# Kernel optimization log

Measured on AMD Instinct MI355X. Metric: run time of the kernel, lower is better.

Reference implementation:

```python
import jax, jax.numpy as jnp
import numpy as np
import math

IMG = 640.0
SIZES = [32.0, 64.0, 128.0, 256.0]
STRIDES = [4, 8, 16, 32]
ARS = [0.5, 1.0, 2.0]
PRE_TOPK = 1000      # RPN_PRE_NMS_TOPK_TEST
POST_TOPK = 150      # RPN_POST_NMS_TOPK_TEST
NMS_THR = 0.7        # RPN_NMS_THRESHOLD
MIN_SIZE = 4.0       # MIN_BOX_SIZE
BBOX_CLAMP = math.log(1000.0 / 16.0)
ROI_OUT = 7          # ROI_OUTPUT_SIZE


def conv(x, w, b, pad):
    y = jax.lax.conv_general_dilated(x, w, (1, 1), [(pad, pad), (pad, pad)],
                                     dimension_numbers=('NCHW', 'OIHW', 'NCHW'))
    return y + b[None, :, None, None]


def level_anchors(H, W, stride, size):
    sx = (jnp.arange(W, dtype=jnp.float32) + 0.5) * stride
    sy = (jnp.arange(H, dtype=jnp.float32) + 0.5) * stride
    SY, SX = jnp.meshgrid(sy, sx, indexing='ij')
    shifts = jnp.stack([SX, SY, SX, SY], axis=-1).reshape(-1, 4)  # [H*W,4]
    base = []
    area = size * size
    for ar in ARS:
        w = math.sqrt(area / ar)
        h = ar * w
        base.append([-w / 2.0, -h / 2.0, w / 2.0, h / 2.0])
    base = jnp.asarray(base, jnp.float32)  # [3,4]
    return (shifts[:, None, :] + base[None, :, :]).reshape(-1, 4)  # [H*W*3,4]


def decode(deltas, boxes):
    w = jnp.maximum(boxes[:, 2] - boxes[:, 0], 1e-6)
    h = jnp.maximum(boxes[:, 3] - boxes[:, 1], 1e-6)
    cx = boxes[:, 0] + 0.5 * w
    cy = boxes[:, 1] + 0.5 * h
    dx, dy = deltas[:, 0], deltas[:, 1]
    dw = jnp.minimum(deltas[:, 2], BBOX_CLAMP)
    dh = jnp.minimum(deltas[:, 3], BBOX_CLAMP)
    pcx = cx + dx * w
    pcy = cy + dy * h
    pw = w * jnp.exp(dw)
    ph = h * jnp.exp(dh)
    return jnp.stack([pcx - 0.5 * pw, pcy - 0.5 * ph, pcx + 0.5 * pw, pcy + 0.5 * ph], axis=1)


def pairwise_iou(b):
    area = jnp.maximum(b[:, 2] - b[:, 0], 0) * jnp.maximum(b[:, 3] - b[:, 1], 0)
    lt = jnp.maximum(b[:, None, :2], b[None, :, :2])
    rb = jnp.minimum(b[:, None, 2:], b[None, :, 2:])
    wh = jnp.maximum(rb - lt, 0.0)
    inter = wh[..., 0] * wh[..., 1]
    return inter / jnp.maximum(area[:, None] + area[None, :] - inter, 1e-6)


def roi_align(feat, boxes, scale):
    # feat [C,H,W]; boxes [R,4] in image coords; one bilinear sample per bin center
    C, H, W = feat.shape
    b = boxes * scale
    x1, y1, x2, y2 = b[:, 0], b[:, 1], b[:, 2], b[:, 3]
    bw = jnp.maximum(x2 - x1, 1.0)
    bh = jnp.maximum(y2 - y1, 1.0)
    g = (jnp.arange(ROI_OUT, dtype=jnp.float32) + 0.5) / ROI_OUT
    px = x1[:, None] + g[None, :] * bw[:, None]   # [R,7]
    py = y1[:, None] + g[None, :] * bh[:, None]
    Y = jnp.broadcast_to(py[:, :, None], (py.shape[0], ROI_OUT, ROI_OUT))
    X = jnp.broadcast_to(px[:, None, :], (px.shape[0], ROI_OUT, ROI_OUT))
    y0f = jnp.floor(Y)
    x0f = jnp.floor(X)
    ly = Y - y0f
    lx = X - x0f
    y0 = jnp.clip(y0f, 0, H - 1).astype(jnp.int32)
    y1i = jnp.clip(y0f + 1, 0, H - 1).astype(jnp.int32)
    x0 = jnp.clip(x0f, 0, W - 1).astype(jnp.int32)
    x1i = jnp.clip(x0f + 1, 0, W - 1).astype(jnp.int32)
    f = lambda yi, xi: feat[:, yi, xi]  # [C,R,7,7]
    val = (f(y0, x0) * (1 - ly) * (1 - lx) + f(y0, x1i) * (1 - ly) * lx
           + f(y1i, x0) * ly * (1 - lx) + f(y1i, x1i) * ly * lx)
    return val.transpose(1, 0, 2, 3)  # [R,C,7,7]


def _forward(p2, p3, p4, p5, rpn_conv_w, rpn_conv_b, obj_w, obj_b, delta_w, delta_b,
             fc1_w, fc1_b, fc2_w, fc2_b, cls_w, cls_b, bbox_w, bbox_b):
    feats = [p2, p3, p4, p5]
    all_boxes, all_scores, all_lvl = [], [], []
    for lvl, (feat, stride, size) in enumerate(zip(feats, STRIDES, SIZES)):
        hid = jax.nn.relu(conv(feat, rpn_conv_w, rpn_conv_b, 1))
        obj = conv(hid, obj_w, obj_b, 0)      # [1,3,H,W]
        dlt = conv(hid, delta_w, delta_b, 0)  # [1,12,H,W]
        _, A, H, W = obj.shape
        scores = obj.transpose(0, 2, 3, 1).reshape(-1)  # [H*W*3]
        deltas = dlt.reshape(1, A, 4, H, W).transpose(0, 3, 4, 1, 2).reshape(-1, 4)
        anchors = level_anchors(H, W, stride, size)
        top_s, idx = jax.lax.top_k(scores, PRE_TOPK)
        boxes = jnp.clip(decode(deltas[idx], anchors[idx]), 0.0, IMG - 1.0)
        ww = boxes[:, 2] - boxes[:, 0]
        hh = boxes[:, 3] - boxes[:, 1]
        valid = (ww >= MIN_SIZE) & (hh >= MIN_SIZE)
        all_boxes.append(boxes)
        all_scores.append(jnp.where(valid, top_s, -1e30))
        all_lvl.append(jnp.full((PRE_TOPK,), float(lvl), jnp.float32))
    boxes = jnp.concatenate(all_boxes)   # [4000,4]
    scores = jnp.concatenate(all_scores)
    lvls = jnp.concatenate(all_lvl)
    N = boxes.shape[0]
    order = jnp.argsort(-scores)
    boxes_s = boxes[order]
    scores_s = scores[order]
    lvl_s = lvls[order]
    # batched NMS: offset per level so different levels never suppress each other
    off_boxes = boxes_s + (lvl_s * (IMG + 1.0) * 2.0)[:, None]
    iou = pairwise_iou(off_boxes)
    idx_r = jnp.arange(N)

    def body(i, keep):
        sup = (iou[i] > NMS_THR) & (idx_r > i) & keep[i]
        return keep & (~sup)

    keep = jax.lax.fori_loop(0, N, body, jnp.ones((N,), bool))
    kept_scores = jnp.where(keep, scores_s, -1e30)
    _, top_idx = jax.lax.top_k(kept_scores, POST_TOPK)
    props = boxes_s[top_idx]  # [150,4]
    # FPN level assignment (canonical formula) for ROI pooling
    pw = jnp.maximum(props[:, 2] - props[:, 0], 0.0)
    ph = jnp.maximum(props[:, 3] - props[:, 1], 0.0)
    k = jnp.clip(jnp.floor(4.0 + jnp.log2(jnp.sqrt(pw * ph) / 224.0 + 1e-6)), 2, 5)
    pooled = jnp.zeros((POST_TOPK, p2.shape[1], ROI_OUT, ROI_OUT), props.dtype)
    for lvl, (feat, stride) in enumerate(zip(feats, STRIDES)):
        pl = roi_align(feat[0], props, 1.0 / stride)
        pooled = pooled + jnp.where((k == (lvl + 2))[:, None, None, None], pl, 0.0)
    x = pooled.reshape(POST_TOPK, -1)            # [150, 12544]
    x = jax.nn.relu(x @ fc1_w.T + fc1_b)
    x = jax.nn.relu(x @ fc2_w.T + fc2_b)
    cls = x @ cls_w.T + cls_b                    # [150, 21]
    bbx = x @ bbox_w.T + bbox_b                  # [150, 84]
    return jnp.concatenate([cls, bbx], axis=-1)  # [150, 105]


def setup_inputs() -> dict:
    key = jax.random.key(0)
    ks = jax.random.split(key, 14)
    C = 256
    rn = lambda k, shape, s: jax.random.normal(k, shape, jnp.float32) * s
    return {
        'p2': rn(ks[0], (1, C, 160, 160), 0.5),
        'p3': rn(ks[1], (1, C, 80, 80), 0.5),
        'p4': rn(ks[2], (1, C, 40, 40), 0.5),
        'p5': rn(ks[3], (1, C, 20, 20), 0.5),
        'rpn_conv_w': rn(ks[4], (C, C, 3, 3), 0.01),
        'rpn_conv_b': jnp.zeros((C,), jnp.float32),
        'obj_w': rn(ks[5], (3, C, 1, 1), 0.01),
        'obj_b': jnp.zeros((3,), jnp.float32),
        'delta_w': rn(ks[6], (12, C, 1, 1), 0.01),
        'delta_b': jnp.zeros((12,), jnp.float32),
        'fc1_w': rn(ks[7], (1024, C * ROI_OUT * ROI_OUT), 0.01),
        'fc1_b': jnp.zeros((1024,), jnp.float32),
        'fc2_w': rn(ks[8], (1024, 1024), 0.01),
        'fc2_b': jnp.zeros((1024,), jnp.float32),
        'cls_w': rn(ks[9], (21, 1024), 0.01),
        'cls_b': jnp.zeros((21,), jnp.float32),
        'bbox_w': rn(ks[10], (84, 1024), 0.001),
        'bbox_b': jnp.zeros((84,), jnp.float32),
    }


def reference(p2, p3, p4, p5, rpn_conv_w, rpn_conv_b, obj_w, obj_b, delta_w, delta_b,
              fc1_w, fc1_b, fc2_w, fc2_b, cls_w, cls_b, bbox_w, bbox_b):
    return _forward(p2, p3, p4, p5, rpn_conv_w, rpn_conv_b, obj_w, obj_b, delta_w, delta_b,
                    fc1_w, fc1_b, fc2_w, fc2_b, cls_w, cls_b, bbox_w, bbox_b)
```

## Files before the change

kernel.cpp:

```cpp
#include <hip/hip_runtime.h>
#include <cstdint>

typedef unsigned long long u64;
typedef unsigned int u32;

__device__ inline u32 fmono(float f){ u32 u = __float_as_uint(f); u32 m = (u & 0x80000000u) ? 0xFFFFFFFFu : 0x80000000u; return u ^ m; }

__device__ const int    g_H[4]       = {160, 80, 40, 20};
__device__ const int    g_strideI[4] = {4, 8, 16, 32};
__device__ const float  g_size[4]    = {32.f, 64.f, 128.f, 256.f};
__device__ const int    g_cofs[4]    = {0, 76800, 96000, 100800};
__device__ const int    g_cnt[4]     = {76800, 19200, 4800, 1200};
__device__ const int    c_blkBase[5] = {0, 1600, 2000, 2288, 2416};
__device__ const int    c_S[4]       = {4, 4, 8, 8};
__device__ const int    c_pofs[4]    = {0, 25600, 32000, 33600};
__device__ const size_t c_partofs[4] = {0, 26214400, 32768000, 36044800};

__global__ __launch_bounds__(256) void wtr_k(const float* __restrict__ w, float* __restrict__ wT){
  __shared__ float tile[32][33];
  int tx = threadIdx.x & 31, ty = threadIdx.x >> 5;
  int row0 = blockIdx.x*32, co0 = blockIdx.y*32;
  #pragma unroll
  for (int r=0;r<4;r++){
    int co = co0 + ty + r*8;
    tile[ty+r*8][tx] = w[(size_t)co*2304 + row0 + tx];
  }
  __syncthreads();
  #pragma unroll
  for (int r=0;r<4;r++){
    int row = row0 + ty + r*8;
    wT[(size_t)row*256 + co0 + tx] = tile[tx][ty+r*8];
  }
}

__global__ void wcat_k(const float* __restrict__ cls_w, const float* __restrict__ cls_b,
                       const float* __restrict__ bbox_w, const float* __restrict__ bbox_b,
                       float* __restrict__ wcat, float* __restrict__ bcat){
  int t = blockIdx.x*256 + threadIdx.x;
  if (t < 105*1024){ int o = t >> 10, k = t & 1023; wcat[t] = (o < 21) ? cls_w[o*1024+k] : bbox_w[(o-21)*1024+k]; }
  if (t < 105) bcat[t] = (t < 21) ? cls_b[t] : bbox_b[t-21];
}

#define KC 4
__global__ __launch_bounds__(256) void rpn_conv_all_k(
    const float* __restrict__ p0, const float* __restrict__ p1,
    const float* __restrict__ p2f, const float* __restrict__ p3f,
    const float* __restrict__ wT, const float* __restrict__ bias,
    float* __restrict__ hid, float* __restrict__ convp)
{
  int bid = blockIdx.x;
  int lvl = (bid >= c_blkBase[1]) + (bid >= c_blkBase[2]) + (bid >= c_blkBase[3]);
  int local = bid - c_blkBase[lvl];
  int nz  = c_S[lvl];
  int H = g_H[lvl], W = H;
  const float* in = (lvl==0)?p0:((lvl==1)?p1:((lvl==2)?p2f:p3f));
  float* part = convp + c_partofs[lvl];
  int zb   = local % nz;
  int cb   = (local / nz) & 3;
  int tile = local / (nz*4);

  int tilesX = (W + 15) >> 4;
  int tr0 = (tile / tilesX) * 16;
  int tc0 = (tile % tilesX) * 16;
  int ciPer = 256 / nz;
  int ciBeg = zb * ciPer;
  int t   = threadIdx.x;
  int tco = t & 15, tp = t >> 4;
  int pr = (tp >> 2) * 4, pc = (tp & 3) * 4;
  int HW = H*W;

  __shared__ float sIn[KC][18][20];
  __shared__ float sW[KC*9][64];

  float* sInF = &sIn[0][0][0];
  float* sWF  = &sW[0][0];

  int   iOff[6]; int iLds[6]; bool iOk[6];
  #pragma unroll
  for (int s=0;s<6;s++){
    int e = t + s*256;
    bool a = (s<5) || (t < (KC*324 - 5*256));
    int ee = a ? e : 0;
    int c = ee/324, r2 = ee%324, row = r2/18, col = r2%18;
    int gy = tr0+row-1, gx = tc0+col-1;
    bool ok = a && ((unsigned)gy < (unsigned)H) && ((unsigned)gx < (unsigned)W);
    iOff[s] = c*HW + gy*W + gx;
    iLds[s] = c*360 + row*20 + col;
    iOk[s]  = ok;
  }
  bool iAct5 = (t < (KC*324 - 5*256));
  int wOff[3]; int wLds[3];
  #pragma unroll
  for (int s=0;s<3;s++){
    int e4 = t + s*256;
    bool a = (s<2) || (t < (KC*9*16 - 2*256));
    int ee = a ? e4 : 0;
    int row = ee>>4, c4 = (ee&15)<<2;
    wOff[s] = row*256 + cb*64 + c4;
    wLds[s] = row*64 + c4;
  }
  bool wAct2 = (t < (KC*9*16 - 2*256));

  float acc[4][16];
  #pragma unroll
  for (int o=0;o<4;o++)
    #pragma unroll
    for (int p=0;p<16;p++) acc[o][p]=0.f;

  float  ri0,ri1,ri2,ri3,ri4,ri5;
  float4 rw0,rw1,rw2;

  {
    const float* inb = in + (size_t)ciBeg*HW;
    const float* wb  = wT + (size_t)ciBeg*2304;
    ri0 = iOk[0] ? inb[iOff[0]] : 0.f;
    ri1 = iOk[1] ? inb[iOff[1]] : 0.f;
    ri2 = iOk[2] ? inb[iOff[2]] : 0.f;
    ri3 = iOk[3] ? inb[iOff[3]] : 0.f;
    ri4 = iOk[4] ? inb[iOff[4]] : 0.f;
    ri5 = iOk[5] ? inb[iOff[5]] : 0.f;
    rw0 = *(const float4*)&wb[wOff[0]];
    rw1 = *(const float4*)&wb[wOff[1]];
    if (wAct2) rw2 = *(const float4*)&wb[wOff[2]];
  }

  int ciEnd = ciBeg + ciPer;
  for (int ci0=ciBeg; ci0<ciEnd; ci0+=KC){
    sInF[iLds[0]] = ri0; sInF[iLds[1]] = ri1; sInF[iLds[2]] = ri2;
    sInF[iLds[3]] = ri3; sInF[iLds[4]] = ri4;
    if (iAct5) sInF[iLds[5]] = ri5;
    *(float4*)&sWF[wLds[0]] = rw0;
    *(float4*)&sWF[wLds[1]] = rw1;
    if (wAct2) *(float4*)&sWF[wLds[2]] = rw2;
    __syncthreads();

    if (ci0 + KC < ciEnd){
      const float* inb = in + (size_t)(ci0+KC)*HW;
      const float* wb  = wT + (size_t)(ci0+KC)*2304;
      ri0 = iOk[0] ? inb[iOff[0]] : 0.f;
      ri1 = iOk[1] ? inb[iOff[1]] : 0.f;
      ri2 = iOk[2] ? inb[iOff[2]] : 0.f;
      ri3 = iOk[3] ? inb[iOff[3]] : 0.f;
      ri4 = iOk[4] ? inb[iOff[4]] : 0.f;
      ri5 = iOk[5] ? inb[iOff[5]] : 0.f;
      rw0 = *(const float4*)&wb[wOff[0]];
      rw1 = *(const float4*)&wb[wOff[1]];
      if (wAct2) rw2 = *(const float4*)&wb[wOff[2]];
    }

    #pragma unroll
    for (int c=0;c<KC;c++){
      float rin[6][6];
      #pragma unroll
      for (int rr=0;rr<6;rr++){
        float4 a = *(const float4*)&sIn[c][pr+rr][pc];
        float2 b = *(const float2*)&sIn[c][pr+rr][pc+4];
        rin[rr][0]=a.x; rin[rr][1]=a.y; rin[rr][2]=a.z; rin[rr][3]=a.w;
        rin[rr][4]=b.x; rin[rr][5]=b.y;
      }
      #pragma unroll
      for (int k=0;k<9;k++){
        int ky=k/3, kx=k%3;
        float4 w0 = *(const float4*)&sW[c*9+k][tco*4];
        float wv[4] = {w0.x,w0.y,w0.z,w0.w};
        #pragma unroll
        for (int dr=0;dr<4;dr++)
          #pragma unroll
          for (int dc=0;dc<4;dc++){
            float iv = rin[dr+ky][dc+kx];
            int p = dr*4+dc;
            #pragma unroll
            for (int o=0;o<4;o++) acc[o][p] = fmaf(wv[o], iv, acc[o][p]);
          }
      }
    }
    __syncthreads();
  }

  int coBase = cb*64 + tco*4;
  float* pb = part + (size_t)zb*HW*256;
  #pragma unroll
  for (int dr=0;dr<4;dr++){
    int gy = tr0+pr+dr; if (gy>=H) continue;
    #pragma unroll
    for (int dc=0;dc<4;dc++){
      int gx = tc0+pc+dc; if (gx>=W) continue;
      int p = dr*4+dc;
      *(float4*)&pb[(size_t)(gy*W+gx)*256 + coBase] = make_float4(acc[0][p],acc[1][p],acc[2][p],acc[3][p]);
    }
  }
}

__global__ __launch_bounds__(256) void conv_red_all_k(const float* __restrict__ convp,
  const float* __restrict__ bias, float* __restrict__ hid)
{
  int idx = blockIdx.x*256 + threadIdx.x;
  if (idx >= 34000*256) return;
  int lvl = (idx >= 25600*256) + (idx >= 32000*256) + (idx >= 33600*256);
  int S = c_S[lvl];
  size_t base = c_partofs[lvl];
  int local = idx - c_pofs[lvl]*256;
  size_t stride = (size_t)g_H[lvl]*g_H[lvl]*256;
  float v = 0.f;
  for (int s=0;s<S;s++) v += convp[base + (size_t)s*stride + local];
  v += bias[idx & 255];
  hid[idx] = v>0.f ? v : 0.f;
}

__global__ __launch_bounds__(256) void rpn_heads_k(
  const float* __restrict__ hid, const float* __restrict__ ow, const float* __restrict__ ob,
  const float* __restrict__ dw, const float* __restrict__ db,
  float* __restrict__ scores, float* __restrict__ deltas)
{
  __shared__ float sw[15][256];
  int t = threadIdx.x;
  for (int e=t; e<15*256; e+=256){ int o=e>>8, k=e&255; sw[o][k] = (o<3)? ow[o*256+k] : dw[(o-3)*256+k]; }
  __syncthreads();
  int wv = t>>6, lane = t&63;
  #pragma unroll
  for (int i=0;i<16;i++){
    int gpx = blockIdx.x*64 + wv*16 + i;
    if (gpx >= 34000) return;
    float4 v = *(const float4*)&hid[(size_t)gpx*256 + lane*4];
    float a[15];
    #pragma unroll
    for (int o=0;o<15;o++){
      const float* w = &sw[o][lane*4];
      a[o] = w[0]*v.x + w[1]*v.y + w[2]*v.z + w[3]*v.w;
    }
    #pragma unroll
    for (int off=32; off; off>>=1)
      #pragma unroll
      for (int o=0;o<15;o++) a[o] += __shfl_xor(a[o], off, 64);
    if (lane==0){
      for (int q=0;q<3;q++) scores[gpx*3+q] = a[q] + ob[q];
      for (int q=0;q<3;q++)
        for (int j=0;j<4;j++)
          deltas[(size_t)(gpx*3+q)*4 + j] = a[3+q*4+j] + db[q*4+j];
    }
  }
}

__global__ __launch_bounds__(1024) void topk_k(
  const float* __restrict__ scores, float* __restrict__ top_s, u32* __restrict__ top_idx)
{
  int lvl = blockIdx.x;
  int base = g_cofs[lvl], N = g_cnt[lvl];
  const int K = 1000;
  __shared__ u64 sbuf[1024];
  u32* hist = (u32*)sbuf;
  __shared__ u64 shT; __shared__ int shKr; __shared__ int scnt;
  int t = threadIdx.x;
  u64 prefix = 0; int Kr = K;
  const int shifts[6] = {53,42,31,20,9,0};
  const int nbits[6]  = {11,11,11,11,11,9};
  for (int r=0;r<6;r++){
    int shift = shifts[r], nb = nbits[r];
    for (int e=t; e<2048; e+=1024) hist[e]=0;
    __syncthreads();
    int hs = shift + nb;
    for (int e=t; e<N; e+=1024){
      u64 key = ((u64)fmono(scores[base+e]) << 32) | (u32)(~(u32)e);
      bool match = (r==0) || ((key>>hs) == (prefix>>hs));
      if (match) atomicAdd(&hist[(u32)(key>>shift) & ((1u<<nb)-1u)], 1u);
    }
    __syncthreads();
    if (t==0){
      int accu=0, nbin=1<<nb;
      for (int d=nbin-1; d>=0; --d){
        int c = (int)hist[d];
        if (accu + c >= Kr){ shT = prefix | ((u64)d << shift); shKr = Kr - accu; break; }
        accu += c;
      }
    }
    __syncthreads();
    prefix = shT; Kr = shKr;
    __syncthreads();
  }
  sbuf[t] = 0;
  if (t==0) scnt = 0;
  __syncthreads();
  for (int e=t; e<N; e+=1024){
    u64 key = ((u64)fmono(scores[base+e]) << 32) | (u32)(~(u32)e);
    if (key >= prefix){ int p = atomicAdd(&scnt,1); if (p < 1024) sbuf[p]=key; }
  }
  __syncthreads();
  for (int k=2;k<=1024;k<<=1)
    for (int j=k>>1;j>0;j>>=1){
      int i = t, ixj = i^j;
      if (ixj > i){
        u64 x = sbuf[i], y = sbuf[ixj];
        bool up = ((i & k) == 0);
        bool swp = up ? (x<y) : (x>y);
        if (swp){ sbuf[i]=y; sbuf[ixj]=x; }
      }
      __syncthreads();
    }
  if (t<K){
    u64 key = sbuf[t];
    u32 idx = ~((u32)key);
    top_idx[lvl*1000+t] = idx;
    top_s[lvl*1000+t]   = scores[base + (int)idx];
  }
}

__global__ void decode_k(const u32* __restrict__ top_idx, const float* __restrict__ top_s,
                         const float* __restrict__ deltas,
                         float* __restrict__ cat_scores, float4* __restrict__ cat_boxes)
{
  int t = blockIdx.x*256 + threadIdx.x;
  if (t >= 4000) return;
  int lvl = t/1000;
  u32 idx = top_idx[t];
  float score = top_s[t];
  int W = g_H[lvl];
  int strd = g_strideI[lvl];
  float size = g_size[lvl];
  int a = (int)(idx % 3u); int pix = (int)(idx / 3u);
  int px = pix % W, py = pix / W;
  double area = (double)size*(double)size;
  double ar = (a==0)?0.5:((a==1)?1.0:2.0);
  double wd = sqrt(area/ar);
  double hd = ar*wd;
  float bx1 = (float)(-wd*0.5), by1 = (float)(-hd*0.5), bx2=(float)(wd*0.5), by2=(float)(hd*0.5);
  float sx = ((float)px + 0.5f)*(float)strd;
  float sy = ((float)py + 0.5f)*(float)strd;
  float ax1 = sx+bx1, ay1=sy+by1, ax2=sx+bx2, ay2=sy+by2;
  float w = fmaxf(ax2-ax1, 1e-6f), h = fmaxf(ay2-ay1, 1e-6f);
  float cx = ax1 + 0.5f*w, cy = ay1 + 0.5f*h;
  const float* d = &deltas[(size_t)(g_cofs[lvl] + (int)idx)*4];
  float dx = d[0], dy = d[1];
  float dwv = fminf(d[2], 4.135166556742356f);
  float dhv = fminf(d[3], 4.135166556742356f);
  float pcx = cx + dx*w, pcy = cy + dy*h;
  float pw = w*expf(dwv), ph = h*expf(dhv);
  float x1 = pcx - 0.5f*pw, y1 = pcy - 0.5f*ph, x2 = pcx + 0.5f*pw, y2 = pcy + 0.5f*ph;
  x1 = fminf(fmaxf(x1,0.f),639.f); y1 = fminf(fmaxf(y1,0.f),639.f);
  x2 = fminf(fmaxf(x2,0.f),639.f); y2 = fminf(fmaxf(y2,0.f),639.f);
  bool valid = ((x2-x1) >= 4.f) && ((y2-y1) >= 4.f);
  cat_boxes[t] = make_float4(x1,y1,x2,y2);
  cat_scores[t] = valid ? score : -1e30f;
}

__global__ __launch_bounds__(1024) void sort_k(const float* __restrict__ cat_scores, const float4* __restrict__ cat_boxes,
  float* __restrict__ scores_s, float4* __restrict__ boxes_s, float4* __restrict__ obox)
{
  __shared__ u64 s[4096];
  int t = threadIdx.x;
  for (int i=t;i<4096;i+=1024){
    u64 key = 0;
    if (i<4000) key = ((u64)fmono(cat_scores[i])<<32) | (u32)(~(u32)i);
    s[i]=key;
  }
  __syncthreads();
  for (int k=2;k<=4096;k<<=1)
    for (int j=k>>1;j>0;j>>=1){
      for (int i=t;i<4096;i+=1024){
        int ixj=i^j;
        if (ixj>i){
          u64 x=s[i], y=s[ixj];
          bool up = ((i&k)==0);
          bool swp = up ? (x<y):(x>y);
          if (swp){ s[i]=y; s[ixj]=x; }
        }
      }
      __syncthreads();
    }
  for (int r=t;r<4000;r+=1024){
    u32 o = ~((u32)s[r]);
    float4 b = cat_boxes[o];
    scores_s[r] = cat_scores[o];
    boxes_s[r] = b;
    float off = (float)(o/1000u) * 1282.0f;
    obox[r] = make_float4(b.x+off, b.y+off, b.z+off, b.w+off);
  }
}

__global__ __launch_bounds__(256) void iou_k(const float4* __restrict__ obox, u64* __restrict__ mask)
{
  int w = threadIdx.x;
  int i = blockIdx.x*4 + threadIdx.y;
  if (i >= 4000 || w >= 63) return;
  float4 bi = obox[i];
  float ai = fmaxf(bi.z-bi.x,0.f)*fmaxf(bi.w-bi.y,0.f);
  u64 bits=0;
  int c0=w*64;
  for (int l=0;l<64;l++){
    int c=c0+l;
    if (c>=4000) break;
    if (c<=i) continue;
    float4 bc = obox[c];
    float ac = fmaxf(bc.z-bc.x,0.f)*fmaxf(bc.w-bc.y,0.f);
    float ltx = fmaxf(bi.x, bc.x), lty = fmaxf(bi.y, bc.y);
    float rbx = fminf(bi.z, bc.z), rby = fminf(bi.w, bc.w);
    float wx = fmaxf(rbx-ltx,0.f), wy = fmaxf(rby-lty,0.f);
    float inter = wx*wy;
    float uni = fmaxf(ai+ac-inter, 1e-6f);
    if (inter/uni > 0.7f) bits |= (1ull<<l);
  }
  mask[(size_t)i*63 + w] = bits;
}

#define PF 32
__global__ __launch_bounds__(64) void nms_scan_k(const u64* __restrict__ mask,
   const float* __restrict__ scores_s, const float4* __restrict__ boxes_s, float4* __restrict__ props)
{
  int lane = threadIdx.x;
  bool act = lane < 63;
  const u64* mrow = mask + lane;
  u64 removed = 0;

  u64 bufA[PF], bufB[PF];
  #pragma unroll
  for (int j=0;j<PF;j++) bufA[j] = act ? mrow[(size_t)j*63] : 0ull;

  const int NG = 4000/PF;
  for (int g=0; g<NG; g+=2){
    if (g+1 < NG){
      #pragma unroll
      for (int j=0;j<PF;j++) bufB[j] = act ? mrow[(size_t)((g+1)*PF+j)*63] : 0ull;
    }
    #pragma unroll
    for (int j=0;j<PF;j++){
      int i = g*PF + j;
      u64 rm = __shfl(removed, i>>6, 64);
      bool keep = ((rm >> (i&63)) & 1ull) == 0ull;
      if (keep) removed |= bufA[j];
    }
    if (g+2 < NG){
      #pragma unroll
      for (int j=0;j<PF;j++) bufA[j] = act ? mrow[(size_t)((g+2)*PF+j)*63] : 0ull;
    }
    if (g+1 < NG){
      #pragma unroll
      for (int j=0;j<PF;j++){
        int i = (g+1)*PF + j;
        u64 rm = __shfl(removed, i>>6, 64);
        bool keep = ((rm >> (i&63)) & 1ull) == 0ull;
        if (keep) removed |= bufB[j];
      }
    }
  }

  u64 keepbits = ~removed;
  u64 selbits = 0;
  if (act){
    #pragma unroll
    for (int j=0;j<64;j++){
      int i = lane*64 + j;
      if (i < 4000 && ((keepbits>>j)&1ull) && scores_s[i] > -1e29f) selbits |= (1ull<<j);
    }
  }
  u64 validbits = 0;
  if (act){
    int nvalid = 4000 - lane*64;
    if (nvalid >= 64) validbits = ~0ull;
    else if (nvalid > 0) validbits = (1ull<<nvalid) - 1ull;
  }
  u64 nonbits = (~selbits) & validbits;

  int cntSel = __popcll(selbits);
  int incS = cntSel;
  #pragma unroll
  for (int off2=1; off2<64; off2<<=1){ int v = __shfl_up(incS, off2, 64); if (lane>=off2) incS += v; }
  int exSel = incS - cntSel;
  int totalSel = __shfl(incS, 63, 64);
  int cnt = totalSel < 150 ? totalSel : 150;

  int cntNon = __popcll(nonbits);
  int incN = cntNon;
  #pragma unroll
  for (int off2=1; off2<64; off2<<=1){ int v = __shfl_up(incN, off2, 64); if (lane>=off2) incN += v; }
  int exNon = incN - cntNon;

  if (act){
    int r = exSel;
    #pragma unroll
    for (int j=0;j<64;j++){
      if ((selbits>>j)&1ull){
        if (r < 150) props[r] = boxes_s[lane*64 + j];
        r++;
      }
    }
    int r2 = cnt + exNon;
    #pragma unroll
    for (int j=0;j<64;j++){
      if ((nonbits>>j)&1ull){
        if (r2 < 150) props[r2] = boxes_s[lane*64 + j];
        r2++;
      }
    }
  }
}

__global__ __launch_bounds__(256) void roi_k(const float* __restrict__ p2, const float* __restrict__ p3,
  const float* __restrict__ p4, const float* __restrict__ p5, const float4* __restrict__ props, float* __restrict__ x0)
{
  int roi = blockIdx.y, p = blockIdx.x, c = threadIdx.x;
  float4 b = props[roi];
  float pw = fmaxf(b.z-b.x, 0.f), ph = fmaxf(b.w-b.y, 0.f);
  float kf = floorf(4.f + log2f(sqrtf(pw*ph)/224.f + 1e-6f));
  kf = fminf(fmaxf(kf, 2.f), 5.f);
  int lvl = (int)kf - 2;
  const float* f = (lvl==0)?p2:((lvl==1)?p3:((lvl==2)?p4:p5));
  int H = g_H[lvl]; int HW = H*H;
  float scale = 1.f/(float)g_strideI[lvl];
  float x1 = b.x*scale, y1 = b.y*scale, x2 = b.z*scale, y2 = b.w*scale;
  float bw = fmaxf(x2-x1, 1.f), bh = fmaxf(y2-y1, 1.f);
  int py = p/7, px = p%7;
  float gx = ((float)px + 0.5f)/7.f;
  float gy = ((float)py + 0.5f)/7.f;
  float X = x1 + gx*bw;
  float Y = y1 + gy*bh;
  float x0f = floorf(X), y0f = floorf(Y);
  float lx = X - x0f, ly = Y - y0f;
  int xi0 = (int)fminf(fmaxf(x0f,0.f),(float)(H-1));
  int xi1 = (int)fminf(fmaxf(x0f+1.f,0.f),(float)(H-1));
  int yi0 = (int)fminf(fmaxf(y0f,0.f),(float)(H-1));
  int yi1 = (int)fminf(fmaxf(y0f+1.f,0.f),(float)(H-1));
  float v00 = f[(size_t)c*HW + yi0*H + xi0];
  float v01 = f[(size_t)c*HW + yi0*H + xi1];
  float v10 = f[(size_t)c*HW + yi1*H + xi0];
  float v11 = f[(size_t)c*HW + yi1*H + xi1];
  float val = v00*(1.f-ly)*(1.f-lx) + v01*(1.f-ly)*lx + v10*ly*(1.f-lx) + v11*ly*lx;
  x0[(size_t)roi*12544 + c*49 + p] = val;
}

__global__ __launch_bounds__(256) void fc_split_k(const float* __restrict__ X, const float* __restrict__ Wt,
  float* __restrict__ partial, int M, int N, int K, int KS)
{
  __shared__ float sx[32][33];
  __shared__ float sw[32][64];
  int t = threadIdx.x;
  int tn = t & 15, tm = t >> 4;
  int nb = blockIdx.x, mb = blockIdx.y, zb = blockIdx.z;
  int row0 = mb*32 + tm*2, col0 = nb*64 + tn*4;
  int kbeg = zb*KS, kend = kbeg + KS;
  float acc[2][4] = {{0,0,0,0},{0,0,0,0}};
  int wn = t & 63, kg = t >> 6;
  for (int k0=kbeg;k0<kend;k0+=32){
    for (int e=t;e<1024;e+=256){
      int m=e>>5, kk=e&31;
      int row=mb*32+m;
      sx[m][kk] = (row<M)? X[(size_t)row*K + k0+kk] : 0.f;
    }
    int co = nb*64+wn;
    if (co<N){
      const float* wp = &Wt[(size_t)co*K + k0 + kg*8];
      float4 va = *(const float4*)wp;
      float4 vb = *(const float4*)(wp+4);
      sw[kg*8+0][wn]=va.x; sw[kg*8+1][wn]=va.y; sw[kg*8+2][wn]=va.z; sw[kg*8+3][wn]=va.w;
      sw[kg*8+4][wn]=vb.x; sw[kg*8+5][wn]=vb.y; sw[kg*8+6][wn]=vb.z; sw[kg*8+7][wn]=vb.w;
    } else {
      #pragma unroll
      for (int j=0;j<8;j++) sw[kg*8+j][wn]=0.f;
    }
    __syncthreads();
    #pragma unroll 8
    for (int kk=0;kk<32;kk++){
      float xa = sx[tm*2+0][kk], xb = sx[tm*2+1][kk];
      float4 wv = *(const float4*)&sw[kk][tn*4];
      acc[0][0]=fmaf(xa,wv.x,acc[0][0]); acc[0][1]=fmaf(xa,wv.y,acc[0][1]);
      acc[0][2]=fmaf(xa,wv.z,acc[0][2]); acc[0][3]=fmaf(xa,wv.w,acc[0][3]);
      acc[1][0]=fmaf(xb,wv.x,acc[1][0]); acc[1][1]=fmaf(xb,wv.y,acc[1][1]);
      acc[1][2]=fmaf(xb,wv.z,acc[1][2]); acc[1][3]=fmaf(xb,wv.w,acc[1][3]);
    }
    __syncthreads();
  }
  for (int dm=0;dm<2;dm++){
    int row=row0+dm; if (row>=M) continue;
    for (int dn=0;dn<4;dn++){
      int col=col0+dn; if (col>=N) continue;
      partial[((size_t)zb*M + row)*N + col] = acc[dm][dn];
    }
  }
}

__global__ __launch_bounds__(256) void fc_reduce_k(const float* __restrict__ partial, const float* __restrict__ bias,
  float* __restrict__ Y, int M, int N, int S, int dorelu)
{
  int idx = blockIdx.x*256 + threadIdx.x;
  if (idx >= M*N) return;
  int col = idx % N;
  float v = bias[col];
  size_t stride = (size_t)M*N;
  for (int s=0;s<S;s++) v += partial[s*stride + idx];
  if (dorelu) v = fmaxf(v, 0.f);
  Y[idx] = v;
}

extern "C" void kernel_launch(void* const* d_in, const int* in_sizes, int n_in,
                              void* d_out, int out_size, void* d_ws, size_t ws_size,
                              hipStream_t stream)
{
  (void)in_sizes; (void)n_in; (void)out_size; (void)ws_size;
  const float* p[4] = {(const float*)d_in[0], (const float*)d_in[1], (const float*)d_in[2], (const float*)d_in[3]};
  const float* rpn_w = (const float*)d_in[4];
  const float* rpn_b = (const float*)d_in[5];
  const float* obj_w = (const float*)d_in[6];
  const float* obj_b = (const float*)d_in[7];
  const float* del_w = (const float*)d_in[8];
  const float* del_b = (const float*)d_in[9];
  const float* fc1_w = (const float*)d_in[10];
  const float* fc1_b = (const float*)d_in[11];
  const float* fc2_w = (const float*)d_in[12];
  const float* fc2_b = (const float*)d_in[13];
  const float* cls_w = (const float*)d_in[14];
  const float* cls_b = (const float*)d_in[15];
  const float* bbox_w= (const float*)d_in[16];
  const float* bbox_b= (const float*)d_in[17];

  char* ws = (char*)d_ws;
  size_t off = 0;
  auto alloc = [&](size_t bytes){ size_t o = off; off += (bytes + 255) & ~(size_t)255; return o; };
  float*  wT1      = (float*)(ws + alloc(589824ull*4));
  float*  hid      = (float*)(ws + alloc(34000ull*256*4));
  float*  scores   = (float*)(ws + alloc(102000ull*4));
  float*  deltas   = (float*)(ws + alloc(102000ull*16));
  float*  top_s    = (float*)(ws + alloc(4000ull*4));
  u32*    top_idx  = (u32*)  (ws + alloc(4000ull*4));
  float*  cat_sc   = (float*)(ws + alloc(4000ull*4));
  float4* cat_bx   = (float4*)(ws + alloc(4000ull*16));
  float*  scores_s = (float*)(ws + alloc(4000ull*4));
  float4* boxes_s  = (float4*)(ws + alloc(4000ull*16));
  float4* obox     = (float4*)(ws + alloc(4000ull*16));
  u64*    mask     = (u64*)  (ws + alloc(4000ull*63*8));
  float4* props    = (float4*)(ws + alloc(150ull*16));
  float*  x0       = (float*)(ws + alloc(150ull*12544*4));
  float*  x1       = (float*)(ws + alloc(150ull*1024*4));
  float*  x2       = (float*)(ws + alloc(150ull*1024*4));
  float*  wcat     = (float*)(ws + alloc(105ull*1024*4));
  float*  bcat     = (float*)(ws + alloc(105ull*4));
  float*  convp    = (float*)(ws + alloc(36864000ull*4));
  float*  partial  = hid;

  hipLaunchKernelGGL(wtr_k, dim3(72,8), dim3(256), 0, stream, rpn_w, wT1);
  hipLaunchKernelGGL(wcat_k, dim3((105*1024+255)/256), dim3(256), 0, stream, cls_w, cls_b, bbox_w, bbox_b, wcat, bcat);

  hipLaunchKernelGGL(rpn_conv_all_k, dim3(2416), dim3(256), 0, stream,
                     p[0], p[1], p[2], p[3], wT1, rpn_b, hid, convp);
  hipLaunchKernelGGL(conv_red_all_k, dim3(34000), dim3(256), 0, stream, convp, rpn_b, hid);

  hipLaunchKernelGGL(rpn_heads_k, dim3((34000+63)/64), dim3(256), 0, stream,
                     hid, obj_w, obj_b, del_w, del_b, scores, deltas);
  hipLaunchKernelGGL(topk_k, dim3(4), dim3(1024), 0, stream, scores, top_s, top_idx);
  hipLaunchKernelGGL(decode_k, dim3(16), dim3(256), 0, stream, top_idx, top_s, deltas, cat_sc, cat_bx);
  hipLaunchKernelGGL(sort_k, dim3(1), dim3(1024), 0, stream, cat_sc, cat_bx, scores_s, boxes_s, obox);
  hipLaunchKernelGGL(iou_k, dim3(1000), dim3(64,4), 0, stream, obox, mask);
  hipLaunchKernelGGL(nms_scan_k, dim3(1), dim3(64), 0, stream, mask, scores_s, boxes_s, props);
  hipLaunchKernelGGL(roi_k, dim3(49,150), dim3(256), 0, stream, p[0],p[1],p[2],p[3], props, x0);

  hipLaunchKernelGGL(fc_split_k, dim3(16,5,14), dim3(256), 0, stream, x0, fc1_w, partial, 150, 1024, 12544, 896);
  hipLaunchKernelGGL(fc_reduce_k, dim3((150*1024+255)/256), dim3(256), 0, stream, partial, fc1_b, x1, 150, 1024, 14, 1);
  hipLaunchKernelGGL(fc_split_k, dim3(16,5,8), dim3(256), 0, stream, x1, fc2_w, partial, 150, 1024, 1024, 128);
  hipLaunchKernelGGL(fc_reduce_k, dim3((150*1024+255)/256), dim3(256), 0, stream, partial, fc2_b, x2, 150, 1024, 8, 1);
  hipLaunchKernelGGL(fc_split_k, dim3(2,5,8), dim3(256), 0, stream, x2, wcat, partial, 150, 105, 1024, 128);
  hipLaunchKernelGGL(fc_reduce_k, dim3((150*105+255)/256), dim3(256), 0, stream, partial, bcat, (float*)d_out, 150, 105, 8, 0);
}
```

Before: 1.422 ms.

## Fuse conv split-K reduction into RPN heads and simplify top-k selection

```diff
diff --git a/kernel.cpp b/kernel.cpp
--- a/kernel.cpp
+++ b/kernel.cpp
@@ -45,8 +45,7 @@
 __global__ __launch_bounds__(256) void rpn_conv_all_k(
     const float* __restrict__ p0, const float* __restrict__ p1,
     const float* __restrict__ p2f, const float* __restrict__ p3f,
-    const float* __restrict__ wT, const float* __restrict__ bias,
-    float* __restrict__ hid, float* __restrict__ convp)
+    const float* __restrict__ wT, float* __restrict__ convp)
 {
   int bid = blockIdx.x;
   int lvl = (bid >= c_blkBase[1]) + (bid >= c_blkBase[2]) + (bid >= c_blkBase[3]);
@@ -191,24 +190,9 @@
   }
 }
 
-__global__ __launch_bounds__(256) void conv_red_all_k(const float* __restrict__ convp,
-  const float* __restrict__ bias, float* __restrict__ hid)
-{
-  int idx = blockIdx.x*256 + threadIdx.x;
-  if (idx >= 34000*256) return;
-  int lvl = (idx >= 25600*256) + (idx >= 32000*256) + (idx >= 33600*256);
-  int S = c_S[lvl];
-  size_t base = c_partofs[lvl];
-  int local = idx - c_pofs[lvl]*256;
-  size_t stride = (size_t)g_H[lvl]*g_H[lvl]*256;
-  float v = 0.f;
-  for (int s=0;s<S;s++) v += convp[base + (size_t)s*stride + local];
-  v += bias[idx & 255];
-  hid[idx] = v>0.f ? v : 0.f;
-}
-
 __global__ __launch_bounds__(256) void rpn_heads_k(
-  const float* __restrict__ hid, const float* __restrict__ ow, const float* __restrict__ ob,
+  const float* __restrict__ convp, const float* __restrict__ cbias,
+  const float* __restrict__ ow, const float* __restrict__ ob,
   const float* __restrict__ dw, const float* __restrict__ db,
   float* __restrict__ scores, float* __restrict__ deltas)
 {
@@ -217,16 +201,27 @@
   for (int e=t; e<15*256; e+=256){ int o=e>>8, k=e&255; sw[o][k] = (o<3)? ow[o*256+k] : dw[(o-3)*256+k]; }
   __syncthreads();
   int wv = t>>6, lane = t&63;
+  float4 bv = *(const float4*)&cbias[lane*4];
   #pragma unroll
   for (int i=0;i<16;i++){
     int gpx = blockIdx.x*64 + wv*16 + i;
     if (gpx >= 34000) return;
-    float4 v = *(const float4*)&hid[(size_t)gpx*256 + lane*4];
+    int lvl = (gpx >= 25600) + (gpx >= 32000) + (gpx >= 33600);
+    int S = c_S[lvl];
+    size_t stride = (size_t)g_H[lvl]*g_H[lvl]*256;
+    const float* pb = convp + c_partofs[lvl] + (size_t)(gpx - c_pofs[lvl])*256 + lane*4;
+    float vx=0.f, vy=0.f, vz=0.f, vw=0.f;
+    for (int s=0;s<S;s++){
+      float4 q = *(const float4*)(pb + (size_t)s*stride);
+      vx += q.x; vy += q.y; vz += q.z; vw += q.w;
+    }
+    vx += bv.x; vy += bv.y; vz += bv.z; vw += bv.w;
+    vx = vx>0.f?vx:0.f; vy = vy>0.f?vy:0.f; vz = vz>0.f?vz:0.f; vw = vw>0.f?vw:0.f;
     float a[15];
     #pragma unroll
     for (int o=0;o<15;o++){
       const float* w = &sw[o][lane*4];
-      a[o] = w[0]*v.x + w[1]*v.y + w[2]*v.z + w[3]*v.w;
+      a[o] = w[0]*vx + w[1]*vy + w[2]*vz + w[3]*vw;
     }
     #pragma unroll
     for (int off=32; off; off>>=1)
@@ -247,52 +242,48 @@
   int lvl = blockIdx.x;
   int base = g_cofs[lvl], N = g_cnt[lvl];
   const int K = 1000;
-  __shared__ u64 sbuf[1024];
-  u32* hist = (u32*)sbuf;
-  __shared__ u64 shT; __shared__ int shKr; __shared__ int scnt;
+  __shared__ u32 hist[4096];
+  __shared__ u64 sbuf[4096];
+  __shared__ u32 shThr; __shared__ int scnt;
   int t = threadIdx.x;
-  u64 prefix = 0; int Kr = K;
-  const int shifts[6] = {53,42,31,20,9,0};
-  const int nbits[6]  = {11,11,11,11,11,9};
-  for (int r=0;r<6;r++){
-    int shift = shifts[r], nb = nbits[r];
-    for (int e=t; e<2048; e+=1024) hist[e]=0;
-    __syncthreads();
-    int hs = shift + nb;
-    for (int e=t; e<N; e+=1024){
-      u64 key = ((u64)fmono(scores[base+e]) << 32) | (u32)(~(u32)e);
-      bool match = (r==0) || ((key>>hs) == (prefix>>hs));
-      if (match) atomicAdd(&hist[(u32)(key>>shift) & ((1u<<nb)-1u)], 1u);
-    }
-    __syncthreads();
-    if (t==0){
-      int accu=0, nbin=1<<nb;
-      for (int d=nbin-1; d>=0; --d){
-        int c = (int)hist[d];
-        if (accu + c >= Kr){ shT = prefix | ((u64)d << shift); shKr = Kr - accu; break; }
-        accu += c;
-      }
-    }
-    __syncthreads();
-    prefix = shT; Kr = shKr;
-    __syncthreads();
-  }
-  sbuf[t] = 0;
-  if (t==0) scnt = 0;
+  for (int e=t; e<4096; e+=1024) hist[e]=0;
   __syncthreads();
   for (int e=t; e<N; e+=1024){
-    u64 key = ((u64)fmono(scores[base+e]) << 32) | (u32)(~(u32)e);
-    if (key >= prefix){ int p = atomicAdd(&scnt,1); if (p < 1024) sbuf[p]=key; }
-  }
-  __syncthreads();
-  for (int k=2;k<=1024;k<<=1)
+    u32 m = fmono(scores[base+e]);
+    atomicAdd(&hist[m>>20], 1u);
+  }
+  __syncthreads();
+  if (t==0){
+    int accu=0;
+    for (int d=4095; d>=0; --d){
+      int c = (int)hist[d];
+      if (accu + c >= K){ shThr = (u32)d; break; }
+      accu += c;
+    }
+    scnt = 0;
+  }
+  __syncthreads();
+  u32 thr = shThr;
+  for (int e=t; e<4096; e+=1024) sbuf[e]=0ull;
+  __syncthreads();
+  for (int e=t; e<N; e+=1024){
+    u32 m = fmono(scores[base+e]);
+    if ((m>>20) >= thr){
+      int p = atomicAdd(&scnt, 1);
+      if (p < 4096) sbuf[p] = ((u64)m << 32) | (u32)(~(u32)e);
+    }
+  }
+  __syncthreads();
+  for (int k=2;k<=4096;k<<=1)
     for (int j=k>>1;j>0;j>>=1){
-      int i = t, ixj = i^j;
-      if (ixj > i){
-        u64 x = sbuf[i], y = sbuf[ixj];
-        bool up = ((i & k) == 0);
-        bool swp = up ? (x<y) : (x>y);
-        if (swp){ sbuf[i]=y; sbuf[ixj]=x; }
+      for (int i=t;i<4096;i+=1024){
+        int ixj = i^j;
+        if (ixj > i){
+          u64 x = sbuf[i], y = sbuf[ixj];
+          bool up = ((i & k) == 0);
+          bool swp = up ? (x<y) : (x>y);
+          if (swp){ sbuf[i]=y; sbuf[ixj]=x; }
+        }
       }
       __syncthreads();
     }
@@ -638,11 +629,9 @@
   hipLaunchKernelGGL(wcat_k, dim3((105*1024+255)/256), dim3(256), 0, stream, cls_w, cls_b, bbox_w, bbox_b, wcat, bcat);
 
   hipLaunchKernelGGL(rpn_conv_all_k, dim3(2416), dim3(256), 0, stream,
-                     p[0], p[1], p[2], p[3], wT1, rpn_b, hid, convp);
-  hipLaunchKernelGGL(conv_red_all_k, dim3(34000), dim3(256), 0, stream, convp, rpn_b, hid);
-
+                     p[0], p[1], p[2], p[3], wT1, convp);
   hipLaunchKernelGGL(rpn_heads_k, dim3((34000+63)/64), dim3(256), 0, stream,
-                     hid, obj_w, obj_b, del_w, del_b, scores, deltas);
+                     convp, rpn_b, obj_w, obj_b, del_w, del_b, scores, deltas);
   hipLaunchKernelGGL(topk_k, dim3(4), dim3(1024), 0, stream, scores, top_s, top_idx);
   hipLaunchKernelGGL(decode_k, dim3(16), dim3(256), 0, stream, top_idx, top_s, deltas, cat_sc, cat_bx);
   hipLaunchKernelGGL(sort_k, dim3(1), dim3(1024), 0, stream, cat_sc, cat_bx, scores_s, boxes_s, obox);
```

After: 1.352 ms. 4.9% less time.
